# Optimization experiments

Measured on AMD Instinct MI355X. Metric: run time of the kernel, lower is better.

Reference implementation:

```python
import jax, jax.numpy as jnp
import numpy as np

# Standard minigrid color mapping (module references global COLOR_TO_IDX)
COLOR_TO_IDX = {'red': 0, 'green': 1, 'blue': 2, 'purple': 3, 'yellow': 4, 'grey': 5}
AGENT_FEATURE_SIZE = 13
NUM_AGENTS_PER_COLOR = {'grey': 4, 'yellow': 4}
COLOR_ORDER = sorted(NUM_AGENTS_PER_COLOR.keys())  # ['grey', 'yellow']
FEATURE_DIM = 256
B, N = 131072, 16
INPUT_DIM = (1 + sum(NUM_AGENTS_PER_COLOR.values())) * AGENT_FEATURE_SIZE  # 117


def setup_inputs() -> dict:
    key = jax.random.key(0)
    ks = jax.random.split(key, 14)
    inp = {
        'query_position': jax.random.normal(ks[0], (B, 2), jnp.float32),
        'query_direction': jax.random.normal(ks[1], (B, 4), jnp.float32),
        'query_abilities': jax.random.normal(ks[2], (B, 2), jnp.float32),
        'query_carried': jax.random.normal(ks[3], (B, 2), jnp.float32),
        'query_status': jax.random.normal(ks[4], (B, 3), jnp.float32),
        'all_agent_positions': jax.random.normal(ks[5], (B, N, 2), jnp.float32),
        'all_agent_directions': jax.random.normal(ks[6], (B, N, 4), jnp.float32),
        'all_agent_abilities': jax.random.normal(ks[7], (B, N, 2), jnp.float32),
        'all_agent_carried': jax.random.normal(ks[8], (B, N, 2), jnp.float32),
        'all_agent_status': jax.random.normal(ks[9], (B, N, 3), jnp.float32),
        'agent_color_indices': jax.random.randint(ks[10], (B, N), 0, 6, jnp.int32),
        # fc params; W stored (in, out) so y = x @ W + b (same math as torch Linear)
        'W': jax.random.normal(ks[11], (INPUT_DIM, FEATURE_DIM), jnp.float32) / np.sqrt(INPUT_DIM),
        'b': jax.random.normal(ks[12], (FEATURE_DIM,), jnp.float32) * 0.01,
    }
    return inp


def reference(query_position, query_direction, query_abilities, query_carried,
              query_status, all_agent_positions, all_agent_directions,
              all_agent_abilities, all_agent_carried, all_agent_status,
              agent_color_indices, W, b):
    batch = query_position.shape[0]
    # (B, N, 13) per-agent features, (B, 13) query features
    F = jnp.concatenate([all_agent_positions, all_agent_directions,
                         all_agent_abilities, all_agent_carried,
                         all_agent_status], axis=-1)
    query = jnp.concatenate([query_position, query_direction, query_abilities,
                             query_carried, query_status], axis=-1)
    feats = [query]
    rows = jnp.arange(batch)[:, None]  # (B, 1) for batched scatter
    for color in COLOR_ORDER:
        cidx = COLOR_TO_IDX[color]
        M = NUM_AGENTS_PER_COLOR[color]
        mask = agent_color_indices == cidx                 # (B, N)
        rank = jnp.cumsum(mask, axis=1) - 1                # slot of each matching agent
        valid = mask & (rank < M)
        slot = jnp.where(valid, rank, M)                   # dump overflow/non-match into slot M
        out = jnp.zeros((batch, M + 1, AGENT_FEATURE_SIZE), F.dtype)
        out = out.at[rows, slot].set(F)                    # unique (b, slot) per valid agent
        feats.append(out[:, :M].reshape(batch, M * AGENT_FEATURE_SIZE))
    x = jnp.concatenate(feats, axis=1)                     # (B, 117)
    return jax.nn.relu(x @ W + b)
```

## Files before the change

kernel.cpp:

```cpp
#include <hip/hip_runtime.h>


#define TM 128
#define XS_LD 136
#define THREADS 512
#define NCOL 256
#define GRIDMAX 512

typedef short short8 __attribute__((ext_vector_type(8)));
typedef float f32x4 __attribute__((ext_vector_type(4)));

__device__ __forceinline__ short f2bf(float x) {
    unsigned u = __builtin_bit_cast(unsigned, x);
    unsigned r = (u + 0x7fffu + ((u >> 16) & 1u)) >> 16;
    return (short)r;
}
__device__ __forceinline__ unsigned pk2(float a, float b) {
    return (unsigned)(unsigned short)f2bf(a) | ((unsigned)(unsigned short)f2bf(b) << 16);
}

__global__ __launch_bounds__(256)
void swz_w_kernel(const float* __restrict__ W, short* __restrict__ Wb) {
    const int idx  = blockIdx.x * 256 + threadIdx.x;
    const int j    = idx & 7;
    const int lane = (idx >> 3) & 63;
    const int ct   = (idx >> 9) & 3;
    const int kt   = (idx >> 11) & 3;
    const int cg   = (idx >> 13) & 3;
    const int kk   = kt * 32 + (lane >> 4) * 8 + j;
    const int u    = kk / 14;
    const int f    = kk - u * 14;
    const int col  = cg * 64 + ct * 16 + (lane & 15);
    float v = 0.f;
    if (u < 9 && f < 13) v = W[(u * 13 + f) * NCOL + col];
    Wb[idx] = f2bf(v);
}

template<bool WS>
__global__ __launch_bounds__(THREADS, 4)
void mga_encoder_kernel(const float* __restrict__ qpos, const float* __restrict__ qdir,
                        const float* __restrict__ qabil, const float* __restrict__ qcarr,
                        const float* __restrict__ qstat,
                        const float* __restrict__ apos, const float* __restrict__ adir,
                        const float* __restrict__ aabil, const float* __restrict__ acarr,
                        const float* __restrict__ astat,
                        const int* __restrict__ cidx,
                        const float* __restrict__ W, const float* __restrict__ bvec,
                        const short* __restrict__ Wb,
                        float* __restrict__ out, int nchunks) {
    __shared__ __align__(16) short Xs[TM * XS_LD];

    const int tid  = threadIdx.x;
    const int wave = tid >> 6;
    const int lane = tid & 63;
    const int ln   = lane & 15;
    const int q    = lane >> 4;
    const int r0w  = (wave & 1) * 64;
    const int cg   = wave >> 1;
    const int c0   = cg * 64;

    #pragma unroll
    for (int i = tid; i < TM * 5; i += THREADS) {
        const int row = i / 5, w = i - row * 5;
        *(unsigned*)&Xs[row * XS_LD + 126 + w * 2] = 0u;
    }

    const int rr  = tid >> 4;
    const int u   = tid & 15;
    const int grp = tid & 48;

    const short8* Wf = (const short8*)Wb;

    #pragma unroll 1
    for (int t = blockIdx.x; t < nchunks; t += gridDim.x) {
        const int rowbase = t * TM;

        if (tid < TM) {
            const size_t b = (size_t)(rowbase + tid);
            const float2 qp = ((const float2*)qpos)[b];
            const float4 qd = ((const float4*)qdir)[b];
            const float2 qa = ((const float2*)qabil)[b];
            const float2 qc = ((const float2*)qcarr)[b];
            const float s0 = qstat[b * 3 + 0];
            const float s1 = qstat[b * 3 + 1];
            const float s2 = qstat[b * 3 + 2];
            unsigned* xd = (unsigned*)&Xs[tid * XS_LD];
            xd[0] = pk2(qp.x, qp.y); xd[1] = pk2(qd.x, qd.y);
            xd[2] = pk2(qd.z, qd.w); xd[3] = pk2(qa.x, qa.y);
            xd[4] = pk2(qc.x, qc.y); xd[5] = pk2(s0, s1);
            xd[6] = pk2(s2, 0.f);
        }

        int cs[4];
        #pragma unroll
        for (int p = 0; p < 4; p++)
            cs[p] = cidx[((size_t)(rowbase + p * 32 + rr)) * 16 + u];

        #pragma unroll
        for (int p = 0; p < 4; p++) {
            const int r = p * 32 + rr;
            const size_t b = (size_t)(rowbase + r);
            const int c = cs[p];
            const unsigned long long bg = __ballot(c == 5);
            const unsigned long long by = __ballot(c == 4);
            if (u >= 1 && u <= 8) {
                unsigned mm = (unsigned)(((u <= 4) ? bg : by) >> grp) & 0xFFFFu;
                const int rank = (u - 1) & 3;
                mm = (rank > 0) ? (mm & (mm - 1)) : mm;
                mm = (rank > 1) ? (mm & (mm - 1)) : mm;
                mm = (rank > 2) ? (mm & (mm - 1)) : mm;
                const int j = mm ? (__ffs(mm) - 1) : -1;
                float f0=0.f,f1=0.f,f2=0.f,f3=0.f,f4=0.f,f5=0.f,f6=0.f,
                      f7=0.f,f8=0.f,f9=0.f,f10=0.f,f11=0.f,f12=0.f;
                if (j >= 0) {
                    const size_t a = b * 16 + (size_t)j;
                    const float2 pp = ((const float2*)apos)[a];
                    const float4 dd = ((const float4*)adir)[a];
                    const float2 ab = ((const float2*)aabil)[a];
                    const float2 ca = ((const float2*)acarr)[a];
                    f0 = pp.x; f1 = pp.y;
                    f2 = dd.x; f3 = dd.y; f4 = dd.z; f5 = dd.w;
                    f6 = ab.x; f7 = ab.y; f8 = ca.x; f9 = ca.y;
                    f10 = astat[a * 3 + 0]; f11 = astat[a * 3 + 1]; f12 = astat[a * 3 + 2];
                }
                unsigned* xd = (unsigned*)&Xs[r * XS_LD + 14 * u];
                xd[0] = pk2(f0, f1);   xd[1] = pk2(f2, f3);
                xd[2] = pk2(f4, f5);   xd[3] = pk2(f6, f7);
                xd[4] = pk2(f8, f9);   xd[5] = pk2(f10, f11);
                xd[6] = pk2(f12, 0.f);
            }
        }
        __syncthreads();

        #pragma unroll 1
        for (int h = 0; h < 2; h++) {
            short8 bfr[4][2];
            if constexpr (WS) {
                #pragma unroll
                for (int kt = 0; kt < 4; kt++)
                    #pragma unroll
                    for (int cc = 0; cc < 2; cc++)
                        bfr[kt][cc] = Wf[((cg * 4 + kt) * 4 + 2 * h + cc) * 64 + lane];
            } else {
                #pragma unroll
                for (int kt = 0; kt < 4; kt++)
                    #pragma unroll
                    for (int cc = 0; cc < 2; cc++) {
                        short8 fr;
                        #pragma unroll
                        for (int j = 0; j < 8; j++) {
                            const int kk = kt * 32 + q * 8 + j;
                            const int uu = kk / 14;
                            const int ff = kk - uu * 14;
                            float v = 0.f;
                            if (uu < 9 && ff < 13)
                                v = W[(uu * 13 + ff) * NCOL + c0 + (2 * h + cc) * 16 + ln];
                            fr[j] = f2bf(v);
                        }
                        bfr[kt][cc] = fr;
                    }
            }
            f32x4 bv[2];
            #pragma unroll
            for (int cc = 0; cc < 2; cc++)
                bv[cc] = *(const f32x4*)&bvec[c0 + (2 * h + cc) * 16 + q * 4];

            f32x4 acc[4][2];
            #pragma unroll
            for (int rt = 0; rt < 4; rt++)
                #pragma unroll
                for (int cc = 0; cc < 2; cc++) acc[rt][cc] = (f32x4){0.f, 0.f, 0.f, 0.f};

            #pragma unroll
            for (int kt = 0; kt < 4; kt++) {
                short8 av[4];
                #pragma unroll
                for (int rt = 0; rt < 4; rt++)
                    av[rt] = *(const short8*)&Xs[(r0w + rt * 16 + ln) * XS_LD + kt * 32 + q * 8];
                #pragma unroll
                for (int rt = 0; rt < 4; rt++)
                    #pragma unroll
                    for (int cc = 0; cc < 2; cc++)
                        acc[rt][cc] = __builtin_amdgcn_mfma_f32_16x16x32_bf16(
                            bfr[kt][cc], av[rt], acc[rt][cc], 0, 0, 0);
            }

            #pragma unroll
            for (int rt = 0; rt < 4; rt++) {
                const int row = rowbase + r0w + rt * 16 + ln;
                #pragma unroll
                for (int cc = 0; cc < 2; cc++) {
                    const int col = c0 + (2 * h + cc) * 16 + q * 4;
                    f32x4 v;
                    v[0] = fmaxf(acc[rt][cc][0] + bv[cc][0], 0.f);
                    v[1] = fmaxf(acc[rt][cc][1] + bv[cc][1], 0.f);
                    v[2] = fmaxf(acc[rt][cc][2] + bv[cc][2], 0.f);
                    v[3] = fmaxf(acc[rt][cc][3] + bv[cc][3], 0.f);
                    __builtin_nontemporal_store(v, (f32x4*)&out[(size_t)row * NCOL + col]);
                }
            }
        }
        __syncthreads();
    }
}

extern "C" void kernel_launch(void* const* d_in, const int* in_sizes, int n_in,
                              void* d_out, int out_size, void* d_ws, size_t ws_size,
                              hipStream_t stream) {
    const float* qpos  = (const float*)d_in[0];
    const float* qdir  = (const float*)d_in[1];
    const float* qabil = (const float*)d_in[2];
    const float* qcarr = (const float*)d_in[3];
    const float* qstat = (const float*)d_in[4];
    const float* apos  = (const float*)d_in[5];
    const float* adir  = (const float*)d_in[6];
    const float* aabil = (const float*)d_in[7];
    const float* acarr = (const float*)d_in[8];
    const float* astat = (const float*)d_in[9];
    const int*   cidx  = (const int*)d_in[10];
    const float* W     = (const float*)d_in[11];
    const float* bvec  = (const float*)d_in[12];
    float* out = (float*)d_out;

    const int B = in_sizes[0] / 2;
    const int nchunks = B / TM;
    const int grid = nchunks < GRIDMAX ? nchunks : GRIDMAX;

    const bool ws_ok = (d_ws != nullptr) && (ws_size >= 32768 * sizeof(short));
    if (ws_ok) {
        swz_w_kernel<<<128, 256, 0, stream>>>(W, (short*)d_ws);
        mga_encoder_kernel<true><<<grid, THREADS, 0, stream>>>(
            qpos, qdir, qabil, qcarr, qstat, apos, adir, aabil, acarr, astat,
            cidx, W, bvec, (const short*)d_ws, out, nchunks);
    } else {
        mga_encoder_kernel<false><<<grid, THREADS, 0, stream>>>(
            qpos, qdir, qabil, qcarr, qstat, apos, adir, aabil, acarr, astat,
            cidx, W, bvec, nullptr, out, nchunks);
    }
}
```

Baseline: 284.4 us.

## Launch one block per row tile instead of persistent grid-stride loop

Replaces the persistent grid-stride loop (grid capped at 512) with one block per 128-row tile, so 1024 blocks launch and the trailing barrier goes away. The launch bound rises from 4 to 8 waves-per-EU hint to allow more resident blocks, and the query-row gather is folded into the u==0 lanes of the agent gather loop. Output stores switch from nontemporal to plain stores. This trades per-block setup (LDS pad zeroing, weight fragment loads) repeated per tile for more latency hiding through occupancy, and the tighter register budget could cause spills.

```diff
diff --git a/kernel.cpp b/kernel.cpp
--- a/kernel.cpp
+++ b/kernel.cpp
@@ -5,7 +5,6 @@
 #define XS_LD 136
 #define THREADS 512
 #define NCOL 256
-#define GRIDMAX 512
 
 typedef short short8 __attribute__((ext_vector_type(8)));
 typedef float f32x4 __attribute__((ext_vector_type(4)));
@@ -37,7 +36,7 @@
 }
 
 template<bool WS>
-__global__ __launch_bounds__(THREADS, 4)
+__global__ __launch_bounds__(THREADS, 8)
 void mga_encoder_kernel(const float* __restrict__ qpos, const float* __restrict__ qdir,
                         const float* __restrict__ qabil, const float* __restrict__ qcarr,
                         const float* __restrict__ qstat,
@@ -47,7 +46,7 @@
                         const int* __restrict__ cidx,
                         const float* __restrict__ W, const float* __restrict__ bvec,
                         const short* __restrict__ Wb,
-                        float* __restrict__ out, int nchunks) {
+                        float* __restrict__ out) {
     __shared__ __align__(16) short Xs[TM * XS_LD];
 
     const int tid  = threadIdx.x;
@@ -58,6 +57,7 @@
     const int r0w  = (wave & 1) * 64;
     const int cg   = wave >> 1;
     const int c0   = cg * 64;
+    const int rowbase = blockIdx.x * TM;
 
     #pragma unroll
     for (int i = tid; i < TM * 5; i += THREADS) {
@@ -69,49 +69,38 @@
     const int u   = tid & 15;
     const int grp = tid & 48;
 
-    const short8* Wf = (const short8*)Wb;
-
-    #pragma unroll 1
-    for (int t = blockIdx.x; t < nchunks; t += gridDim.x) {
-        const int rowbase = t * TM;
-
-        if (tid < TM) {
-            const size_t b = (size_t)(rowbase + tid);
-            const float2 qp = ((const float2*)qpos)[b];
-            const float4 qd = ((const float4*)qdir)[b];
-            const float2 qa = ((const float2*)qabil)[b];
-            const float2 qc = ((const float2*)qcarr)[b];
-            const float s0 = qstat[b * 3 + 0];
-            const float s1 = qstat[b * 3 + 1];
-            const float s2 = qstat[b * 3 + 2];
-            unsigned* xd = (unsigned*)&Xs[tid * XS_LD];
-            xd[0] = pk2(qp.x, qp.y); xd[1] = pk2(qd.x, qd.y);
-            xd[2] = pk2(qd.z, qd.w); xd[3] = pk2(qa.x, qa.y);
-            xd[4] = pk2(qc.x, qc.y); xd[5] = pk2(s0, s1);
-            xd[6] = pk2(s2, 0.f);
-        }
-
-        int cs[4];
-        #pragma unroll
-        for (int p = 0; p < 4; p++)
-            cs[p] = cidx[((size_t)(rowbase + p * 32 + rr)) * 16 + u];
-
-        #pragma unroll
-        for (int p = 0; p < 4; p++) {
-            const int r = p * 32 + rr;
-            const size_t b = (size_t)(rowbase + r);
-            const int c = cs[p];
-            const unsigned long long bg = __ballot(c == 5);
-            const unsigned long long by = __ballot(c == 4);
-            if (u >= 1 && u <= 8) {
+    int cs[4];
+    #pragma unroll
+    for (int p = 0; p < 4; p++)
+        cs[p] = cidx[((size_t)(rowbase + p * 32 + rr)) * 16 + u];
+
+    #pragma unroll
+    for (int p = 0; p < 4; p++) {
+        const int r = p * 32 + rr;
+        const size_t b = (size_t)(rowbase + r);
+        const int c = cs[p];
+        const unsigned long long bg = __ballot(c == 5);
+        const unsigned long long by = __ballot(c == 4);
+        if (u <= 8) {
+            float f0=0.f,f1=0.f,f2=0.f,f3=0.f,f4=0.f,f5=0.f,f6=0.f,
+                  f7=0.f,f8=0.f,f9=0.f,f10=0.f,f11=0.f,f12=0.f;
+            if (u == 0) {
+                const float2 qp = ((const float2*)qpos)[b];
+                const float4 qd = ((const float4*)qdir)[b];
+                const float2 qa = ((const float2*)qabil)[b];
+                const float2 qc = ((const float2*)qcarr)[b];
+                f0 = qp.x; f1 = qp.y;
+                f2 = qd.x; f3 = qd.y; f4 = qd.z; f5 = qd.w;
+                f6 = qa.x; f7 = qa.y;
+                f8 = qc.x; f9 = qc.y;
+                f10 = qstat[b * 3 + 0]; f11 = qstat[b * 3 + 1]; f12 = qstat[b * 3 + 2];
+            } else {
                 unsigned mm = (unsigned)(((u <= 4) ? bg : by) >> grp) & 0xFFFFu;
                 const int rank = (u - 1) & 3;
                 mm = (rank > 0) ? (mm & (mm - 1)) : mm;
                 mm = (rank > 1) ? (mm & (mm - 1)) : mm;
                 mm = (rank > 2) ? (mm & (mm - 1)) : mm;
                 const int j = mm ? (__ffs(mm) - 1) : -1;
-                float f0=0.f,f1=0.f,f2=0.f,f3=0.f,f4=0.f,f5=0.f,f6=0.f,
-                      f7=0.f,f8=0.f,f9=0.f,f10=0.f,f11=0.f,f12=0.f;
                 if (j >= 0) {
                     const size_t a = b * 16 + (size_t)j;
                     const float2 pp = ((const float2*)apos)[a];
@@ -123,84 +112,84 @@
                     f6 = ab.x; f7 = ab.y; f8 = ca.x; f9 = ca.y;
                     f10 = astat[a * 3 + 0]; f11 = astat[a * 3 + 1]; f12 = astat[a * 3 + 2];
                 }
-                unsigned* xd = (unsigned*)&Xs[r * XS_LD + 14 * u];
-                xd[0] = pk2(f0, f1);   xd[1] = pk2(f2, f3);
-                xd[2] = pk2(f4, f5);   xd[3] = pk2(f6, f7);
-                xd[4] = pk2(f8, f9);   xd[5] = pk2(f10, f11);
-                xd[6] = pk2(f12, 0.f);
             }
-        }
-        __syncthreads();
-
-        #pragma unroll 1
-        for (int h = 0; h < 2; h++) {
-            short8 bfr[4][2];
-            if constexpr (WS) {
+            unsigned* xd = (unsigned*)&Xs[r * XS_LD + 14 * u];
+            xd[0] = pk2(f0, f1);   xd[1] = pk2(f2, f3);
+            xd[2] = pk2(f4, f5);   xd[3] = pk2(f6, f7);
+            xd[4] = pk2(f8, f9);   xd[5] = pk2(f10, f11);
+            xd[6] = pk2(f12, 0.f);
+        }
+    }
+    __syncthreads();
+
+    const short8* Wf = (const short8*)Wb;
+    #pragma unroll 1
+    for (int h = 0; h < 2; h++) {
+        short8 bfr[4][2];
+        if constexpr (WS) {
+            #pragma unroll
+            for (int kt = 0; kt < 4; kt++)
                 #pragma unroll
-                for (int kt = 0; kt < 4; kt++)
+                for (int cc = 0; cc < 2; cc++)
+                    bfr[kt][cc] = Wf[((cg * 4 + kt) * 4 + 2 * h + cc) * 64 + lane];
+        } else {
+            #pragma unroll
+            for (int kt = 0; kt < 4; kt++)
+                #pragma unroll
+                for (int cc = 0; cc < 2; cc++) {
+                    short8 fr;
                     #pragma unroll
-                    for (int cc = 0; cc < 2; cc++)
-                        bfr[kt][cc] = Wf[((cg * 4 + kt) * 4 + 2 * h + cc) * 64 + lane];
-            } else {
-                #pragma unroll
-                for (int kt = 0; kt < 4; kt++)
-                    #pragma unroll
-                    for (int cc = 0; cc < 2; cc++) {
-                        short8 fr;
-                        #pragma unroll
-                        for (int j = 0; j < 8; j++) {
-                            const int kk = kt * 32 + q * 8 + j;
-                            const int uu = kk / 14;
-                            const int ff = kk - uu * 14;
-                            float v = 0.f;
-                            if (uu < 9 && ff < 13)
-                                v = W[(uu * 13 + ff) * NCOL + c0 + (2 * h + cc) * 16 + ln];
-                            fr[j] = f2bf(v);
-                        }
-                        bfr[kt][cc] = fr;
+                    for (int j = 0; j < 8; j++) {
+                        const int kk = kt * 32 + q * 8 + j;
+                        const int uu = kk / 14;
+                        const int ff = kk - uu * 14;
+                        float v = 0.f;
+                        if (uu < 9 && ff < 13)
+                            v = W[(uu * 13 + ff) * NCOL + c0 + (2 * h + cc) * 16 + ln];
+                        fr[j] = f2bf(v);
                     }
-            }
-            f32x4 bv[2];
-            #pragma unroll
-            for (int cc = 0; cc < 2; cc++)
-                bv[cc] = *(const f32x4*)&bvec[c0 + (2 * h + cc) * 16 + q * 4];
-
-            f32x4 acc[4][2];
+                    bfr[kt][cc] = fr;
+                }
+        }
+        f32x4 bv[2];
+        #pragma unroll
+        for (int cc = 0; cc < 2; cc++)
+            bv[cc] = *(const f32x4*)&bvec[c0 + (2 * h + cc) * 16 + q * 4];
+
+        f32x4 acc[4][2];
+        #pragma unroll
+        for (int rt = 0; rt < 4; rt++)
+            #pragma unroll
+            for (int cc = 0; cc < 2; cc++) acc[rt][cc] = (f32x4){0.f, 0.f, 0.f, 0.f};
+
+        #pragma unroll
+        for (int kt = 0; kt < 4; kt++) {
+            short8 av[4];
+            #pragma unroll
+            for (int rt = 0; rt < 4; rt++)
+                av[rt] = *(const short8*)&Xs[(r0w + rt * 16 + ln) * XS_LD + kt * 32 + q * 8];
             #pragma unroll
             for (int rt = 0; rt < 4; rt++)
                 #pragma unroll
-                for (int cc = 0; cc < 2; cc++) acc[rt][cc] = (f32x4){0.f, 0.f, 0.f, 0.f};
-
-            #pragma unroll
-            for (int kt = 0; kt < 4; kt++) {
-                short8 av[4];
-                #pragma unroll
-                for (int rt = 0; rt < 4; rt++)
-                    av[rt] = *(const short8*)&Xs[(r0w + rt * 16 + ln) * XS_LD + kt * 32 + q * 8];
-                #pragma unroll
-                for (int rt = 0; rt < 4; rt++)
-                    #pragma unroll
-                    for (int cc = 0; cc < 2; cc++)
-                        acc[rt][cc] = __builtin_amdgcn_mfma_f32_16x16x32_bf16(
-                            bfr[kt][cc], av[rt], acc[rt][cc], 0, 0, 0);
+                for (int cc = 0; cc < 2; cc++)
+                    acc[rt][cc] = __builtin_amdgcn_mfma_f32_16x16x32_bf16(
+                        bfr[kt][cc], av[rt], acc[rt][cc], 0, 0, 0);
+        }
+
+        #pragma unroll
+        for (int rt = 0; rt < 4; rt++) {
+            const int row = rowbase + r0w + rt * 16 + ln;
+            #pragma unroll
+            for (int cc = 0; cc < 2; cc++) {
+                const int col = c0 + (2 * h + cc) * 16 + q * 4;
+                f32x4 v;
+                v[0] = fmaxf(acc[rt][cc][0] + bv[cc][0], 0.f);
+                v[1] = fmaxf(acc[rt][cc][1] + bv[cc][1], 0.f);
+                v[2] = fmaxf(acc[rt][cc][2] + bv[cc][2], 0.f);
+                v[3] = fmaxf(acc[rt][cc][3] + bv[cc][3], 0.f);
+                *(f32x4*)&out[(size_t)row * NCOL + col] = v;
             }
-
-            #pragma unroll
-            for (int rt = 0; rt < 4; rt++) {
-                const int row = rowbase + r0w + rt * 16 + ln;
-                #pragma unroll
-                for (int cc = 0; cc < 2; cc++) {
-                    const int col = c0 + (2 * h + cc) * 16 + q * 4;
-                    f32x4 v;
-                    v[0] = fmaxf(acc[rt][cc][0] + bv[cc][0], 0.f);
-                    v[1] = fmaxf(acc[rt][cc][1] + bv[cc][1], 0.f);
-                    v[2] = fmaxf(acc[rt][cc][2] + bv[cc][2], 0.f);
-                    v[3] = fmaxf(acc[rt][cc][3] + bv[cc][3], 0.f);
-                    __builtin_nontemporal_store(v, (f32x4*)&out[(size_t)row * NCOL + col]);
-                }
-            }
-        }
-        __syncthreads();
+        }
     }
 }
 
@@ -223,18 +212,17 @@
     float* out = (float*)d_out;
 
     const int B = in_sizes[0] / 2;
-    const int nchunks = B / TM;
-    const int grid = nchunks < GRIDMAX ? nchunks : GRIDMAX;
+    const int nblocks = B / TM;
 
     const bool ws_ok = (d_ws != nullptr) && (ws_size >= 32768 * sizeof(short));
     if (ws_ok) {
         swz_w_kernel<<<128, 256, 0, stream>>>(W, (short*)d_ws);
-        mga_encoder_kernel<true><<<grid, THREADS, 0, stream>>>(
+        mga_encoder_kernel<true><<<nblocks, THREADS, 0, stream>>>(
             qpos, qdir, qabil, qcarr, qstat, apos, adir, aabil, acarr, astat,
-            cidx, W, bvec, (const short*)d_ws, out, nchunks);
+            cidx, W, bvec, (const short*)d_ws, out);
     } else {
-        mga_encoder_kernel<false><<<grid, THREADS, 0, stream>>>(
+        mga_encoder_kernel<false><<<nblocks, THREADS, 0, stream>>>(
             qpos, qdir, qabil, qcarr, qstat, apos, adir, aabil, acarr, astat,
-            cidx, W, bvec, nullptr, out, nchunks);
-    }
-}
+            cidx, W, bvec, nullptr, out);
+    }
+}
```

Result: slower. 342.2 us (+20.3%).
